# Kernel tuning notes

Measured on AMD Instinct MI355X. Metric: run time of the kernel, lower is better.

The kernel has to match this reference:

```python
import jax, jax.numpy as jnp
import numpy as np

B, S, LATENT = 256, 64, 20
U_DIM = LATENT // 5            # 4
T_HID, T_DEPTH = 20, 4         # treatment MLP
D_HID, D_DEPTH = 4 * LATENT, 4 # drift MLP (80 hidden)
T_LEN = 41
DT = 0.05
SIGMA, THETA, MU = 0.5, 1.0, 0.0
N = B * S
DIM_AUG = LATENT + 2           # latent + logqp + Tx


def _mlp(x, w_in, b_in, w_h, b_h, w_out, b_out, act):
    # input layer always ReLU (MLPSimple), hidden layers use `act`
    h = jax.nn.relu(x @ w_in.T + b_in)
    for i in range(w_h.shape[0]):
        h = act(h @ w_h[i].T + b_h[i])
    return h @ w_out.T + b_out


def setup_inputs() -> dict:
    key = jax.random.key(0)
    ks = jax.random.split(key, 20)

    def lin(k, out_d, in_d):
        bound = 1.0 / np.sqrt(in_d)
        return jax.random.uniform(k, (out_d, in_d), jnp.float32, -bound, bound)

    def bias(k, out_d, in_d):
        bound = 1.0 / np.sqrt(in_d)
        return jax.random.uniform(k, (out_d,), jnp.float32, -bound, bound)

    return {
        "z_SDE": jax.random.normal(ks[0], (B, S, LATENT), jnp.float32),
        "t": jnp.arange(T_LEN, dtype=jnp.float32) * DT,
        "Tx": jax.random.uniform(ks[1], (B,), jnp.float32),
        "noise": jax.random.normal(ks[2], (T_LEN - 1, N, DIM_AUG), jnp.float32),
        # treatment MLP: 1 -> 20 (ReLU) -> [20->20 ReLU]x4 -> 4
        "tw_in": lin(ks[3], T_HID, 1),
        "tb_in": bias(ks[4], T_HID, 1),
        "tw_h": jnp.stack([lin(jax.random.fold_in(ks[5], i), T_HID, T_HID) for i in range(T_DEPTH)]),
        "tb_h": jnp.stack([bias(jax.random.fold_in(ks[6], i), T_HID, T_HID) for i in range(T_DEPTH)]),
        "tw_out": lin(ks[7], U_DIM, T_HID),
        "tb_out": bias(ks[8], U_DIM, T_HID),
        # drift MLP: 24 -> 80 (ReLU) -> [80->80 Tanh]x4 -> 20
        "dw_in": lin(ks[9], D_HID, LATENT + U_DIM),
        "db_in": bias(ks[10], D_HID, LATENT + U_DIM),
        "dw_h": jnp.stack([lin(jax.random.fold_in(ks[11], i), D_HID, D_HID) for i in range(D_DEPTH)]),
        "db_h": jnp.stack([bias(jax.random.fold_in(ks[12], i), D_HID, D_HID) for i in range(D_DEPTH)]),
        "dw_out": lin(ks[13], LATENT, D_HID),
        "db_out": bias(ks[14], LATENT, D_HID),
    }


def reference(z_SDE, t, Tx, noise, tw_in, tb_in, tw_h, tb_h, tw_out, tb_out,
              dw_in, db_in, dw_h, db_h, dw_out, db_out):
    # build augmented initial state: [z, logqp0=0, Tx]  -> [N, DIM_AUG]
    Tx_rep = jnp.broadcast_to(Tx[:, None, None], (B, S, 1))
    aug_y0 = jnp.concatenate(
        [z_SDE, jnp.zeros((B, S, 1), z_SDE.dtype), Tx_rep.astype(z_SDE.dtype)], axis=-1
    ).reshape(N, DIM_AUG)

    dt = t[1] - t[0]           # 0.05, aligned with euler dt
    sqrt_dt = jnp.sqrt(dt)
    # diagonal diffusion: sigma on latent dims, 0 on (logqp, Tx) aug dims
    g_diag = jnp.concatenate([jnp.full((LATENT,), SIGMA, jnp.float32), jnp.zeros((2,), jnp.float32)])

    def f_aug(ti, y_aug):
        T_ = y_aug[:, -1]                     # treatment indicator
        y = y_aug[:, :LATENT]
        t_col = jnp.broadcast_to(ti, (N, 1)).astype(y.dtype)
        u = _mlp(t_col, tw_in, tb_in, tw_h, tb_h, tw_out, tb_out, jax.nn.relu)
        u_t = u * T_[:, None]
        h = THETA * (MU - y)                  # prior drift
        f = _mlp(jnp.concatenate([y, u_t], axis=-1), dw_in, db_in, dw_h, db_h, dw_out, db_out, jnp.tanh) - h
        # _stable_division(f - h, g); g = sigma = 0.5 > eps so plain division
        uu = (f - h) / SIGMA
        f_logqp = 0.5 * jnp.sum(uu * uu, axis=1, keepdims=True)
        return jnp.concatenate([f, f_logqp, jnp.zeros_like(f_logqp)], axis=1)

    def step(y, inp):
        ti, dW = inp
        y_new = y + f_aug(ti, y) * dt + g_diag[None, :] * (dW * sqrt_dt)
        return y_new, y_new

    _, ys_rest = jax.lax.scan(step, aug_y0, (t[:-1], noise))
    aug_ys = jnp.concatenate([aug_y0[None], ys_rest], axis=0)   # [T, N, DIM_AUG]
    # faithful to source: raw reshape of [T, N, dim] into [B, S, T, dim]
    aug_ys = aug_ys.reshape(-1, S, T_LEN, DIM_AUG)
    ys = aug_ys[:, :, :, :-2]
    logqp = aug_ys[:, :, -1, -2]
    return ys, logqp
```

## Files before the change

kernel.cpp:

```cpp
#include <hip/hip_runtime.h>
#include <math.h>
#include <stdint.h>

#define NPART 16384
#define NSTEP 40
#define DIMA  22
#define OUT0_ELEMS 13434880
#define TRAJ_OFF   160

typedef __attribute__((ext_vector_type(8))) short short8;
typedef __attribute__((ext_vector_type(4))) float floatx4;
typedef __attribute__((ext_vector_type(4))) int   intx4;
typedef __attribute__((ext_vector_type(2))) int   intx2;

union V4 { intx4 i; short8 s; floatx4 f; };

#define AIN_B   0
#define AH_B    5120
#define AOUT_B  56320
#define U_B     61440
#define LDS_BYTES 62080
#define STAGE_DW  15360

__device__ __forceinline__ uint32_t pk2(float a0, float a1) {
    uint32_t r;
    asm("v_cvt_pk_bf16_f32 %0, %1, %2" : "=v"(r) : "v"(a0), "v"(a1));
    return r;
}
__device__ __forceinline__ float fast_tanh(float x) {
    float e = __expf(2.0f * x);
    return 1.0f - 2.0f * __builtin_amdgcn_rcpf(e + 1.0f);
}

__global__ __launch_bounds__(256, 1) void sde_mfma(
    const float* __restrict__ z,      const float* __restrict__ t_arr,
    const float* __restrict__ Tx,     const float* __restrict__ noise,
    const float* __restrict__ dw_in,  const float* __restrict__ db_in,
    const float* __restrict__ dw_h,   const float* __restrict__ db_h,
    const float* __restrict__ dw_out, const float* __restrict__ db_out,
    const float* __restrict__ tw_in,  const float* __restrict__ tb_in,
    const float* __restrict__ tw_h,   const float* __restrict__ tb_h,
    const float* __restrict__ tw_out, const float* __restrict__ tb_out,
    float* __restrict__ out0,         float* __restrict__ traj)
{
    __shared__ __align__(16) uint8_t lds[LDS_BYTES];
    const int tid = threadIdx.x;

    for (int di = tid; di < STAGE_DW; di += 256) {
        uint32_t val = 0u;
        if (di < 1280) {
            int r = di & 255, lane = r >> 2, w = r & 3;
            int m = lane & 15, q = lane >> 4, mt = di >> 8;
            int f = -1;
            if (w < 2)            f = 4 * q + 2 * w;
            else if (q == 0)      f = 16 + 2 * (w - 2);
            else if (q == 1)      f = 20 + 2 * (w - 2);
            if (f >= 0)               val = pk2(dw_in[(mt * 16 + m) * 24 + f],
                                                dw_in[(mt * 16 + m) * 24 + f + 1]);
            else if (q == 2 && w == 2) val = pk2(db_in[mt * 16 + m], 0.f);
        } else if (di < 14080) {
            int q2 = di - 1280, g = q2 / 640, r = q2 % 640;
            int l = g / 5, mt = g % 5;
            int lane, f;
            if (r < 512) {
                int kt = r >> 8, rr = r & 255, w = rr & 3;
                lane = rr >> 2;
                f = 16 * (2 * kt + (w >> 1)) + 4 * (lane >> 4) + 2 * (w & 1);
            } else {
                int rr = r - 512, d = rr & 1;
                lane = rr >> 1;
                f = 64 + 4 * (lane >> 4) + 2 * d;
            }
            int m = lane & 15;
            val = pk2(dw_h[l * 6400 + (mt * 16 + m) * 80 + f],
                      dw_h[l * 6400 + (mt * 16 + m) * 80 + f + 1]);
        } else {
            int q2 = di - 14080, mt = q2 / 640, r = q2 % 640;
            int lane, f;
            if (r < 512) {
                int kt = r >> 8, rr = r & 255, w = rr & 3;
                lane = rr >> 2;
                f = 16 * (2 * kt + (w >> 1)) + 4 * (lane >> 4) + 2 * (w & 1);
            } else {
                int rr = r - 512, d = rr & 1;
                lane = rr >> 1;
                f = 64 + 4 * (lane >> 4) + 2 * d;
            }
            int m = mt * 16 + (lane & 15);
            if (m < 20) val = pk2(dw_out[m * 80 + f], dw_out[m * 80 + f + 1]);
        }
        ((uint32_t*)lds)[di] = val;
    }
    if (tid < NSTEP) {
        float ti = t_arr[tid];
        float hh[20], h2[20];
        #pragma unroll
        for (int j = 0; j < 20; j++) {
            float v = tw_in[j] * ti + tb_in[j];
            hh[j] = v > 0.f ? v : 0.f;
        }
        #pragma unroll
        for (int l = 0; l < 4; l++) {
            #pragma unroll
            for (int j = 0; j < 20; j++) {
                float a = tb_h[l * 20 + j];
                #pragma unroll
                for (int k = 0; k < 20; k++) a += tw_h[(l * 20 + j) * 20 + k] * hh[k];
                h2[j] = a > 0.f ? a : 0.f;
            }
            #pragma unroll
            for (int j = 0; j < 20; j++) hh[j] = h2[j];
        }
        #pragma unroll
        for (int c = 0; c < 4; c++) {
            float a = tb_out[c];
            #pragma unroll
            for (int k = 0; k < 20; k++) a += tw_out[c * 20 + k] * hh[k];
            ((float*)(lds + U_B))[tid * 4 + c] = a;
        }
    }

    const int lane = tid & 63;
    const int n15  = lane & 15;
    const int quad = lane >> 4;
    const int wv   = tid >> 6;
    const int n    = blockIdx.x * 64 + wv * 16 + n15;
    const float Txb = Tx[blockIdx.x];
    const float dtv = t_arr[1] - t_arr[0];
    const float sdt = sqrtf(dtv);
    const float hsdt = 0.5f * sdt;

    __syncthreads();

    V4 aIn[5];
    #pragma unroll
    for (int mt = 0; mt < 5; mt++)
        aIn[mt].i = *(const intx4*)(lds + AIN_B + mt * 1024 + lane * 16);

    V4 aH0[20], aH1[20], aH2[20];
    #pragma unroll
    for (int l = 0; l < 4; l++) {
        #pragma unroll
        for (int mt = 0; mt < 5; mt++) {
            const int g = l * 5 + mt;
            const uint8_t* grp = lds + AH_B + (size_t)g * 2560;
            aH0[g].i = *(const intx4*)(grp + lane * 16);
            aH1[g].i = *(const intx4*)(grp + 1024 + lane * 16);
            intx2 h2 = *(const intx2*)(grp + 2048 + lane * 8);
            uint32_t bd = (quad == 0) ? pk2(db_h[l * 80 + mt * 16 + n15], 0.f) : 0u;
            aH2[g].i = (intx4){h2[0], h2[1], (int)bd, 0};
        }
    }

    V4 aO0[2], aO1[2], aO2[2];
    #pragma unroll
    for (int mt = 0; mt < 2; mt++) {
        const uint8_t* grp = lds + AOUT_B + (size_t)mt * 2560;
        aO0[mt].i = *(const intx4*)(grp + lane * 16);
        aO1[mt].i = *(const intx4*)(grp + 1024 + lane * 16);
        intx2 h2 = *(const intx2*)(grp + 2048 + lane * 8);
        int m = mt * 16 + n15;
        uint32_t bd = (quad == 0 && m < 20) ? pk2(db_out[m], 0.f) : 0u;
        aO2[mt].i = (intx4){h2[0], h2[1], (int)bd, 0};
    }

    const floatx4 zf = {0.f, 0.f, 0.f, 0.f};

    float y0[4], y1[4] = {0.f, 0.f, 0.f, 0.f};
    {
        floatx4 zv = *(const floatx4*)(z + (size_t)n * 20 + quad * 4);
        #pragma unroll
        for (int r = 0; r < 4; r++) y0[r] = zv[r];
        *(floatx4*)(out0 + (size_t)n * 20 + quad * 4) = zv;
        if (quad == 0) {
            floatx4 z2 = *(const floatx4*)(z + (size_t)n * 20 + 16);
            #pragma unroll
            for (int r = 0; r < 4; r++) y1[r] = z2[r];
            *(floatx4*)(out0 + (size_t)n * 20 + 16) = z2;
            traj[n] = 0.f;
        }
    }

    floatx4 dW0n = *(const floatx4*)(noise + ((size_t)0 * NPART + n) * DIMA + quad * 4);
    floatx4 dW1n = *(const floatx4*)(noise + ((size_t)0 * NPART + n) * DIMA + 16);
    floatx4 uvn  = *(const floatx4*)((const float*)(lds + U_B));

    float lq = 0.f;
    for (int i = 0; i < NSTEP; i++) {
        floatx4 dW0 = dW0n, dW1 = dW1n, uv = uvn;
        if (i + 1 < NSTEP) {
            size_t nb2 = ((size_t)(i + 1) * NPART + n) * DIMA;
            dW0n = *(const floatx4*)(noise + nb2 + quad * 4);
            dW1n = *(const floatx4*)(noise + nb2 + 16);
            uvn  = *(const floatx4*)((const float*)(lds + U_B) + (i + 1) * 4);
        }

        float ut0 = uv[0] * Txb, ut1 = uv[1] * Txb;
        float ut2 = uv[2] * Txb, ut3 = uv[3] * Txb;

        V4 bin;
        bin.i[0] = pk2(y0[0], y0[1]);
        bin.i[1] = pk2(y0[2], y0[3]);
        if (quad == 0)      { bin.i[2] = pk2(y1[0], y1[1]); bin.i[3] = pk2(y1[2], y1[3]); }
        else if (quad == 1) { bin.i[2] = pk2(ut0, ut1);     bin.i[3] = pk2(ut2, ut3); }
        else if (quad == 2) { bin.i[2] = 0x00003F80;        bin.i[3] = 0; }
        else                { bin.i[2] = 0;                 bin.i[3] = 0; }

        floatx4 acc[5];
        #pragma unroll
        for (int mt = 0; mt < 5; mt++)
            acc[mt] = __builtin_amdgcn_mfma_f32_16x16x32_bf16(aIn[mt].s, bin.s, zf, 0, 0, 0);
        uint32_t pkA[5][2];
        #pragma unroll
        for (int mt = 0; mt < 5; mt++) {
            pkA[mt][0] = pk2(fmaxf(acc[mt][0], 0.f), fmaxf(acc[mt][1], 0.f));
            pkA[mt][1] = pk2(fmaxf(acc[mt][2], 0.f), fmaxf(acc[mt][3], 0.f));
        }

        #pragma unroll
        for (int l = 0; l < 4; l++) {
            V4 b0, b1, b2;
            b0.i = (intx4){(int)pkA[0][0], (int)pkA[0][1], (int)pkA[1][0], (int)pkA[1][1]};
            b1.i = (intx4){(int)pkA[2][0], (int)pkA[2][1], (int)pkA[3][0], (int)pkA[3][1]};
            b2.i = (intx4){(int)pkA[4][0], (int)pkA[4][1], 0x00003F80, 0};
            #pragma unroll
            for (int mt = 0; mt < 5; mt++) {
                const int g = l * 5 + mt;
                floatx4 c0 = __builtin_amdgcn_mfma_f32_16x16x32_bf16(aH0[g].s, b0.s, zf, 0, 0, 0);
                floatx4 c1 = __builtin_amdgcn_mfma_f32_16x16x32_bf16(aH1[g].s, b1.s, zf, 0, 0, 0);
                floatx4 c2 = __builtin_amdgcn_mfma_f32_16x16x32_bf16(aH2[g].s, b2.s, zf, 0, 0, 0);
                acc[mt] = (c0 + c1) + c2;
            }
            #pragma unroll
            for (int mt = 0; mt < 5; mt++) {
                pkA[mt][0] = pk2(fast_tanh(acc[mt][0]), fast_tanh(acc[mt][1]));
                pkA[mt][1] = pk2(fast_tanh(acc[mt][2]), fast_tanh(acc[mt][3]));
            }
        }

        V4 b0, b1, b2;
        b0.i = (intx4){(int)pkA[0][0], (int)pkA[0][1], (int)pkA[1][0], (int)pkA[1][1]};
        b1.i = (intx4){(int)pkA[2][0], (int)pkA[2][1], (int)pkA[3][0], (int)pkA[3][1]};
        b2.i = (intx4){(int)pkA[4][0], (int)pkA[4][1], 0x00003F80, 0};
        floatx4 oacc[2];
        #pragma unroll
        for (int mt = 0; mt < 2; mt++) {
            floatx4 c0 = __builtin_amdgcn_mfma_f32_16x16x32_bf16(aO0[mt].s, b0.s, zf, 0, 0, 0);
            floatx4 c1 = __builtin_amdgcn_mfma_f32_16x16x32_bf16(aO1[mt].s, b1.s, zf, 0, 0, 0);
            floatx4 c2 = __builtin_amdgcn_mfma_f32_16x16x32_bf16(aO2[mt].s, b2.s, zf, 0, 0, 0);
            oacc[mt] = (c0 + c1) + c2;
        }

        float part = 0.f;
        size_t obase = ((size_t)(i + 1) * NPART + n) * 20;
        floatx4 st;
        #pragma unroll
        for (int r = 0; r < 4; r++) {
            float o = oacc[0][r];
            float y = y0[r];
            float f = o + y;
            float uu = 2.f * o + 4.f * y;
            part += uu * uu;
            y0[r] = y + f * dtv + hsdt * dW0[r];
            st[r] = y0[r];
        }
        *(floatx4*)(out0 + obase + quad * 4) = st;
        if (quad == 0) {
            floatx4 st2;
            #pragma unroll
            for (int r = 0; r < 4; r++) {
                float o = oacc[1][r];
                float y = y1[r];
                float f = o + y;
                float uu = 2.f * o + 4.f * y;
                part += uu * uu;
                y1[r] = y + f * dtv + hsdt * dW1[r];
                st2[r] = y1[r];
            }
            *(floatx4*)(out0 + obase + 16) = st2;
        }
        part += __shfl_xor(part, 16);
        part += __shfl_xor(part, 32);
        lq += 0.5f * part * dtv;
        if (quad == 0) traj[(size_t)(i + 1) * NPART + n] = lq;
    }
}

__global__ void gather_logqp(const float* __restrict__ traj, float* __restrict__ out1) {
    int i = blockIdx.x * 256 + threadIdx.x;
    if (i < NPART) out1[i] = traj[(size_t)41 * i + 40];
}

extern "C" void kernel_launch(void* const* d_in, const int* in_sizes, int n_in,
                              void* d_out, int out_size, void* d_ws, size_t ws_size,
                              hipStream_t stream) {
    const float* z      = (const float*)d_in[0];
    const float* t_arr  = (const float*)d_in[1];
    const float* Tx     = (const float*)d_in[2];
    const float* noise  = (const float*)d_in[3];
    const float* tw_in  = (const float*)d_in[4];
    const float* tb_in  = (const float*)d_in[5];
    const float* tw_h   = (const float*)d_in[6];
    const float* tb_h   = (const float*)d_in[7];
    const float* tw_out = (const float*)d_in[8];
    const float* tb_out = (const float*)d_in[9];
    const float* dw_in  = (const float*)d_in[10];
    const float* db_in  = (const float*)d_in[11];
    const float* dw_h   = (const float*)d_in[12];
    const float* db_h   = (const float*)d_in[13];
    const float* dw_out = (const float*)d_in[14];
    const float* db_out = (const float*)d_in[15];

    float* wsf  = (float*)d_ws;
    float* traj = wsf + TRAJ_OFF;
    float* out0 = (float*)d_out;
    float* out1 = out0 + OUT0_ELEMS;

    hipLaunchKernelGGL(sde_mfma, dim3(256), dim3(256), 0, stream,
                       z, t_arr, Tx, noise, dw_in, db_in, dw_h, db_h,
                       dw_out, db_out, tw_in, tb_in, tw_h, tb_h, tw_out, tb_out,
                       out0, traj);
    hipLaunchKernelGGL(gather_logqp, dim3(64), dim3(256), 0, stream, traj, out1);
}
```

Before: 278.9 us.

## Split each particle group's drift MLP across two cooperating waves via LDS

The block grows from 256 to 512 threads. Each 16-particle group is now served by two waves: one computes 3 of the 5 hidden-output tiles, the other computes 2 tiles plus the output layer and the SDE update. The waves swap packed bf16 activations through double-buffered LDS with a barrier after each layer. The goal is to shorten each wave's serial MFMA and tanh chain and put two waves on each SIMD to hide latency. The cost is extra LDS traffic and six block-wide barriers per time step. MFMA partial sums are also chained through the accumulator instead of being added afterwards.

Result: faster. 254.1 us (-8.9%).

```diff
diff --git a/kernel.cpp b/kernel.cpp
--- a/kernel.cpp
+++ b/kernel.cpp
@@ -22,6 +22,10 @@
 #define LDS_BYTES 62080
 #define STAGE_DW  15360
 
+#define PAIR_STRIDE 6144
+#define ACT1_OFF    2560
+#define BIN_OFF     5120
+
 __device__ __forceinline__ uint32_t pk2(float a0, float a1) {
     uint32_t r;
     asm("v_cvt_pk_bf16_f32 %0, %1, %2" : "=v"(r) : "v"(a0), "v"(a1));
@@ -31,8 +35,21 @@
     float e = __expf(2.0f * x);
     return 1.0f - 2.0f * __builtin_amdgcn_rcpf(e + 1.0f);
 }
-
-__global__ __launch_bounds__(256, 1) void sde_mfma(
+__device__ __forceinline__ void relupk(floatx4 a, uint32_t& d0, uint32_t& d1) {
+    d0 = pk2(fmaxf(a[0], 0.f), fmaxf(a[1], 0.f));
+    d1 = pk2(fmaxf(a[2], 0.f), fmaxf(a[3], 0.f));
+}
+__device__ __forceinline__ void tanhpk(floatx4 a, uint32_t& d0, uint32_t& d1) {
+    d0 = pk2(fast_tanh(a[0]), fast_tanh(a[1]));
+    d1 = pk2(fast_tanh(a[2]), fast_tanh(a[3]));
+}
+__device__ __forceinline__ void pbar() {
+    asm volatile("s_waitcnt lgkmcnt(0)" ::: "memory");
+    __builtin_amdgcn_s_barrier();
+    asm volatile("" ::: "memory");
+}
+
+__global__ __launch_bounds__(512, 2) void sde_mfma(
     const float* __restrict__ z,      const float* __restrict__ t_arr,
     const float* __restrict__ Tx,     const float* __restrict__ noise,
     const float* __restrict__ dw_in,  const float* __restrict__ db_in,
@@ -46,7 +63,7 @@
     __shared__ __align__(16) uint8_t lds[LDS_BYTES];
     const int tid = threadIdx.x;
 
-    for (int di = tid; di < STAGE_DW; di += 256) {
+    for (int di = tid; di < STAGE_DW; di += 512) {
         uint32_t val = 0u;
         if (di < 1280) {
             int r = di & 255, lane = r >> 2, w = r & 3;
@@ -124,50 +141,73 @@
     const int n15  = lane & 15;
     const int quad = lane >> 4;
     const int wv   = tid >> 6;
-    const int n    = blockIdx.x * 64 + wv * 16 + n15;
+    const int pairid = wv & 3;
+    const bool roleB = (wv >= 4);
+    const int n    = blockIdx.x * 64 + pairid * 16 + n15;
     const float Txb = Tx[blockIdx.x];
     const float dtv = t_arr[1] - t_arr[0];
     const float sdt = sqrtf(dtv);
     const float hsdt = 0.5f * sdt;
 
+    uint8_t* const pb   = lds + pairid * PAIR_STRIDE;
+    uint32_t* const act0 = (uint32_t*)pb + lane;
+    uint32_t* const act1 = (uint32_t*)(pb + ACT1_OFF) + lane;
+    uint32_t* const binp = (uint32_t*)(pb + BIN_OFF) + lane;
+
     __syncthreads();
 
-    V4 aIn[5];
-    #pragma unroll
-    for (int mt = 0; mt < 5; mt++)
-        aIn[mt].i = *(const intx4*)(lds + AIN_B + mt * 1024 + lane * 16);
-
-    V4 aH0[20], aH1[20], aH2[20];
-    #pragma unroll
-    for (int l = 0; l < 4; l++) {
-        #pragma unroll
-        for (int mt = 0; mt < 5; mt++) {
-            const int g = l * 5 + mt;
-            const uint8_t* grp = lds + AH_B + (size_t)g * 2560;
+    V4 aIn[3], aH0[12], aH1[12], aH2[12];
+    if (!roleB) {
+        #pragma unroll
+        for (int mt = 0; mt < 3; mt++)
+            aIn[mt].i = *(const intx4*)(lds + AIN_B + mt * 1024 + lane * 16);
+        #pragma unroll
+        for (int l = 0; l < 4; l++) {
+            #pragma unroll
+            for (int mt = 0; mt < 3; mt++) {
+                const uint8_t* grp = lds + AH_B + (size_t)(l * 5 + mt) * 2560;
+                const int g = l * 3 + mt;
+                aH0[g].i = *(const intx4*)(grp + lane * 16);
+                aH1[g].i = *(const intx4*)(grp + 1024 + lane * 16);
+                intx2 h2 = *(const intx2*)(grp + 2048 + lane * 8);
+                uint32_t bd = (quad == 0) ? pk2(db_h[l * 80 + mt * 16 + n15], 0.f) : 0u;
+                aH2[g].i = (intx4){h2[0], h2[1], (int)bd, 0};
+            }
+        }
+    } else {
+        #pragma unroll
+        for (int mt = 0; mt < 2; mt++)
+            aIn[mt].i = *(const intx4*)(lds + AIN_B + (3 + mt) * 1024 + lane * 16);
+        #pragma unroll
+        for (int l = 0; l < 4; l++) {
+            #pragma unroll
+            for (int mt = 0; mt < 2; mt++) {
+                const uint8_t* grp = lds + AH_B + (size_t)(l * 5 + 3 + mt) * 2560;
+                const int g = l * 2 + mt;
+                aH0[g].i = *(const intx4*)(grp + lane * 16);
+                aH1[g].i = *(const intx4*)(grp + 1024 + lane * 16);
+                intx2 h2 = *(const intx2*)(grp + 2048 + lane * 8);
+                uint32_t bd = (quad == 0) ? pk2(db_h[l * 80 + (3 + mt) * 16 + n15], 0.f) : 0u;
+                aH2[g].i = (intx4){h2[0], h2[1], (int)bd, 0};
+            }
+        }
+        #pragma unroll
+        for (int mt = 0; mt < 2; mt++) {
+            const uint8_t* grp = lds + AOUT_B + (size_t)mt * 2560;
+            const int g = 8 + mt;
             aH0[g].i = *(const intx4*)(grp + lane * 16);
             aH1[g].i = *(const intx4*)(grp + 1024 + lane * 16);
             intx2 h2 = *(const intx2*)(grp + 2048 + lane * 8);
-            uint32_t bd = (quad == 0) ? pk2(db_h[l * 80 + mt * 16 + n15], 0.f) : 0u;
+            int m = mt * 16 + n15;
+            uint32_t bd = (quad == 0 && m < 20) ? pk2(db_out[m], 0.f) : 0u;
             aH2[g].i = (intx4){h2[0], h2[1], (int)bd, 0};
         }
     }
 
-    V4 aO0[2], aO1[2], aO2[2];
-    #pragma unroll
-    for (int mt = 0; mt < 2; mt++) {
-        const uint8_t* grp = lds + AOUT_B + (size_t)mt * 2560;
-        aO0[mt].i = *(const intx4*)(grp + lane * 16);
-        aO1[mt].i = *(const intx4*)(grp + 1024 + lane * 16);
-        intx2 h2 = *(const intx2*)(grp + 2048 + lane * 8);
-        int m = mt * 16 + n15;
-        uint32_t bd = (quad == 0 && m < 20) ? pk2(db_out[m], 0.f) : 0u;
-        aO2[mt].i = (intx4){h2[0], h2[1], (int)bd, 0};
-    }
-
-    const floatx4 zf = {0.f, 0.f, 0.f, 0.f};
-
-    float y0[4], y1[4] = {0.f, 0.f, 0.f, 0.f};
-    {
+    float y0[4] = {0.f, 0.f, 0.f, 0.f}, y1[4] = {0.f, 0.f, 0.f, 0.f};
+    V4 binB; binB.i = (intx4){0, 0, 0, 0};
+    float lq = 0.f;
+    if (roleB) {
         floatx4 zv = *(const floatx4*)(z + (size_t)n * 20 + quad * 4);
         #pragma unroll
         for (int r = 0; r < 4; r++) y0[r] = zv[r];
@@ -180,109 +220,164 @@
             traj[n] = 0.f;
         }
     }
-
-    floatx4 dW0n = *(const floatx4*)(noise + ((size_t)0 * NPART + n) * DIMA + quad * 4);
-    floatx4 dW1n = *(const floatx4*)(noise + ((size_t)0 * NPART + n) * DIMA + 16);
-    floatx4 uvn  = *(const floatx4*)((const float*)(lds + U_B));
-
-    float lq = 0.f;
+    __syncthreads();
+
+    if (roleB) {
+        const floatx4 uv0 = *(const floatx4*)((const float*)(lds + U_B));
+        float ut0 = uv0[0] * Txb, ut1 = uv0[1] * Txb;
+        float ut2 = uv0[2] * Txb, ut3 = uv0[3] * Txb;
+        binB.i[0] = pk2(y0[0], y0[1]);
+        binB.i[1] = pk2(y0[2], y0[3]);
+        if (quad == 0)      { binB.i[2] = pk2(y1[0], y1[1]); binB.i[3] = pk2(y1[2], y1[3]); }
+        else if (quad == 1) { binB.i[2] = pk2(ut0, ut1);     binB.i[3] = pk2(ut2, ut3); }
+        else if (quad == 2) { binB.i[2] = 0x00003F80;        binB.i[3] = 0; }
+        else                { binB.i[2] = 0;                 binB.i[3] = 0; }
+        binp[0] = binB.i[0]; binp[64] = binB.i[1];
+        binp[128] = binB.i[2]; binp[192] = binB.i[3];
+    }
+    __syncthreads();
+
+    const floatx4 zf = {0.f, 0.f, 0.f, 0.f};
+    floatx4 dW0 = zf, dW1 = zf, uvn = zf;
+    uint32_t pka[2], pkb[2], pkc[2];
+
     for (int i = 0; i < NSTEP; i++) {
-        floatx4 dW0 = dW0n, dW1 = dW1n, uv = uvn;
-        if (i + 1 < NSTEP) {
-            size_t nb2 = ((size_t)(i + 1) * NPART + n) * DIMA;
-            dW0n = *(const floatx4*)(noise + nb2 + quad * 4);
-            dW1n = *(const floatx4*)(noise + nb2 + 16);
-            uvn  = *(const floatx4*)((const float*)(lds + U_B) + (i + 1) * 4);
-        }
-
-        float ut0 = uv[0] * Txb, ut1 = uv[1] * Txb;
-        float ut2 = uv[2] * Txb, ut3 = uv[3] * Txb;
-
-        V4 bin;
-        bin.i[0] = pk2(y0[0], y0[1]);
-        bin.i[1] = pk2(y0[2], y0[3]);
-        if (quad == 0)      { bin.i[2] = pk2(y1[0], y1[1]); bin.i[3] = pk2(y1[2], y1[3]); }
-        else if (quad == 1) { bin.i[2] = pk2(ut0, ut1);     bin.i[3] = pk2(ut2, ut3); }
-        else if (quad == 2) { bin.i[2] = 0x00003F80;        bin.i[3] = 0; }
-        else                { bin.i[2] = 0;                 bin.i[3] = 0; }
-
-        floatx4 acc[5];
-        #pragma unroll
-        for (int mt = 0; mt < 5; mt++)
-            acc[mt] = __builtin_amdgcn_mfma_f32_16x16x32_bf16(aIn[mt].s, bin.s, zf, 0, 0, 0);
-        uint32_t pkA[5][2];
-        #pragma unroll
-        for (int mt = 0; mt < 5; mt++) {
-            pkA[mt][0] = pk2(fmaxf(acc[mt][0], 0.f), fmaxf(acc[mt][1], 0.f));
-            pkA[mt][1] = pk2(fmaxf(acc[mt][2], 0.f), fmaxf(acc[mt][3], 0.f));
-        }
+        if (roleB) {
+            size_t nb = ((size_t)i * NPART + n) * DIMA;
+            dW0 = *(const floatx4*)(noise + nb + quad * 4);
+            if (quad == 0) dW1 = *(const floatx4*)(noise + nb + 16);
+            int inx = (i + 1 < NSTEP) ? i + 1 : i;
+            uvn = *(const floatx4*)((const float*)(lds + U_B) + inx * 4);
+        }
+
+        if (!roleB) {
+            V4 binA;
+            binA.i = (intx4){(int)binp[0], (int)binp[64], (int)binp[128], (int)binp[192]};
+            floatx4 a0 = __builtin_amdgcn_mfma_f32_16x16x32_bf16(aIn[0].s, binA.s, zf, 0, 0, 0);
+            floatx4 a1 = __builtin_amdgcn_mfma_f32_16x16x32_bf16(aIn[1].s, binA.s, zf, 0, 0, 0);
+            floatx4 a2 = __builtin_amdgcn_mfma_f32_16x16x32_bf16(aIn[2].s, binA.s, zf, 0, 0, 0);
+            relupk(a0, pka[0], pka[1]);
+            relupk(a1, pkb[0], pkb[1]);
+            relupk(a2, pkc[0], pkc[1]);
+            act0[0]   = pka[0]; act0[64]  = pka[1];
+            act0[128] = pkb[0]; act0[192] = pkb[1];
+            act0[256] = pkc[0]; act0[320] = pkc[1];
+        } else {
+            floatx4 a0 = __builtin_amdgcn_mfma_f32_16x16x32_bf16(aIn[0].s, binB.s, zf, 0, 0, 0);
+            floatx4 a1 = __builtin_amdgcn_mfma_f32_16x16x32_bf16(aIn[1].s, binB.s, zf, 0, 0, 0);
+            relupk(a0, pka[0], pka[1]);
+            relupk(a1, pkb[0], pkb[1]);
+            act0[384] = pka[0]; act0[448] = pka[1];
+            act0[512] = pkb[0]; act0[576] = pkb[1];
+        }
+        pbar();
 
         #pragma unroll
         for (int l = 0; l < 4; l++) {
+            uint32_t* rb = (l & 1) ? act1 : act0;
+            uint32_t* wb = (l & 1) ? act0 : act1;
+            if (!roleB) {
+                uint32_t r6 = rb[384], r7 = rb[448], r8 = rb[512], r9 = rb[576];
+                V4 b0, b1, b2;
+                b0.i = (intx4){(int)pka[0], (int)pka[1], (int)pkb[0], (int)pkb[1]};
+                b1.i = (intx4){(int)pkc[0], (int)pkc[1], (int)r6, (int)r7};
+                b2.i = (intx4){(int)r8, (int)r9, 0x00003F80, 0};
+                floatx4 acc[3];
+                #pragma unroll
+                for (int mt = 0; mt < 3; mt++) {
+                    const int g = l * 3 + mt;
+                    floatx4 c = __builtin_amdgcn_mfma_f32_16x16x32_bf16(aH0[g].s, b0.s, zf, 0, 0, 0);
+                    c = __builtin_amdgcn_mfma_f32_16x16x32_bf16(aH1[g].s, b1.s, c, 0, 0, 0);
+                    acc[mt] = __builtin_amdgcn_mfma_f32_16x16x32_bf16(aH2[g].s, b2.s, c, 0, 0, 0);
+                }
+                tanhpk(acc[0], pka[0], pka[1]);
+                tanhpk(acc[1], pkb[0], pkb[1]);
+                tanhpk(acc[2], pkc[0], pkc[1]);
+                wb[0]   = pka[0]; wb[64]  = pka[1];
+                wb[128] = pkb[0]; wb[192] = pkb[1];
+                wb[256] = pkc[0]; wb[320] = pkc[1];
+            } else {
+                uint32_t r0 = rb[0], r1 = rb[64], r2 = rb[128], r3 = rb[192], r4 = rb[256], r5 = rb[320];
+                V4 b0, b1, b2;
+                b0.i = (intx4){(int)r0, (int)r1, (int)r2, (int)r3};
+                b1.i = (intx4){(int)r4, (int)r5, (int)pka[0], (int)pka[1]};
+                b2.i = (intx4){(int)pkb[0], (int)pkb[1], 0x00003F80, 0};
+                floatx4 acc[2];
+                #pragma unroll
+                for (int mt = 0; mt < 2; mt++) {
+                    const int g = l * 2 + mt;
+                    floatx4 c = __builtin_amdgcn_mfma_f32_16x16x32_bf16(aH0[g].s, b0.s, zf, 0, 0, 0);
+                    c = __builtin_amdgcn_mfma_f32_16x16x32_bf16(aH1[g].s, b1.s, c, 0, 0, 0);
+                    acc[mt] = __builtin_amdgcn_mfma_f32_16x16x32_bf16(aH2[g].s, b2.s, c, 0, 0, 0);
+                }
+                tanhpk(acc[0], pka[0], pka[1]);
+                tanhpk(acc[1], pkb[0], pkb[1]);
+                wb[384] = pka[0]; wb[448] = pka[1];
+                wb[512] = pkb[0]; wb[576] = pkb[1];
+            }
+            pbar();
+        }
+
+        if (roleB) {
+            uint32_t r0 = act0[0], r1 = act0[64], r2 = act0[128], r3 = act0[192], r4 = act0[256], r5 = act0[320];
             V4 b0, b1, b2;
-            b0.i = (intx4){(int)pkA[0][0], (int)pkA[0][1], (int)pkA[1][0], (int)pkA[1][1]};
-            b1.i = (intx4){(int)pkA[2][0], (int)pkA[2][1], (int)pkA[3][0], (int)pkA[3][1]};
-            b2.i = (intx4){(int)pkA[4][0], (int)pkA[4][1], 0x00003F80, 0};
-            #pragma unroll
-            for (int mt = 0; mt < 5; mt++) {
-                const int g = l * 5 + mt;
-                floatx4 c0 = __builtin_amdgcn_mfma_f32_16x16x32_bf16(aH0[g].s, b0.s, zf, 0, 0, 0);
-                floatx4 c1 = __builtin_amdgcn_mfma_f32_16x16x32_bf16(aH1[g].s, b1.s, zf, 0, 0, 0);
-                floatx4 c2 = __builtin_amdgcn_mfma_f32_16x16x32_bf16(aH2[g].s, b2.s, zf, 0, 0, 0);
-                acc[mt] = (c0 + c1) + c2;
-            }
-            #pragma unroll
-            for (int mt = 0; mt < 5; mt++) {
-                pkA[mt][0] = pk2(fast_tanh(acc[mt][0]), fast_tanh(acc[mt][1]));
-                pkA[mt][1] = pk2(fast_tanh(acc[mt][2]), fast_tanh(acc[mt][3]));
-            }
-        }
-
-        V4 b0, b1, b2;
-        b0.i = (intx4){(int)pkA[0][0], (int)pkA[0][1], (int)pkA[1][0], (int)pkA[1][1]};
-        b1.i = (intx4){(int)pkA[2][0], (int)pkA[2][1], (int)pkA[3][0], (int)pkA[3][1]};
-        b2.i = (intx4){(int)pkA[4][0], (int)pkA[4][1], 0x00003F80, 0};
-        floatx4 oacc[2];
-        #pragma unroll
-        for (int mt = 0; mt < 2; mt++) {
-            floatx4 c0 = __builtin_amdgcn_mfma_f32_16x16x32_bf16(aO0[mt].s, b0.s, zf, 0, 0, 0);
-            floatx4 c1 = __builtin_amdgcn_mfma_f32_16x16x32_bf16(aO1[mt].s, b1.s, zf, 0, 0, 0);
-            floatx4 c2 = __builtin_amdgcn_mfma_f32_16x16x32_bf16(aO2[mt].s, b2.s, zf, 0, 0, 0);
-            oacc[mt] = (c0 + c1) + c2;
-        }
-
-        float part = 0.f;
-        size_t obase = ((size_t)(i + 1) * NPART + n) * 20;
-        floatx4 st;
-        #pragma unroll
-        for (int r = 0; r < 4; r++) {
-            float o = oacc[0][r];
-            float y = y0[r];
-            float f = o + y;
-            float uu = 2.f * o + 4.f * y;
-            part += uu * uu;
-            y0[r] = y + f * dtv + hsdt * dW0[r];
-            st[r] = y0[r];
-        }
-        *(floatx4*)(out0 + obase + quad * 4) = st;
-        if (quad == 0) {
-            floatx4 st2;
+            b0.i = (intx4){(int)r0, (int)r1, (int)r2, (int)r3};
+            b1.i = (intx4){(int)r4, (int)r5, (int)pka[0], (int)pka[1]};
+            b2.i = (intx4){(int)pkb[0], (int)pkb[1], 0x00003F80, 0};
+            floatx4 oacc[2];
+            #pragma unroll
+            for (int mt = 0; mt < 2; mt++) {
+                const int g = 8 + mt;
+                floatx4 c = __builtin_amdgcn_mfma_f32_16x16x32_bf16(aH0[g].s, b0.s, zf, 0, 0, 0);
+                c = __builtin_amdgcn_mfma_f32_16x16x32_bf16(aH1[g].s, b1.s, c, 0, 0, 0);
+                oacc[mt] = __builtin_amdgcn_mfma_f32_16x16x32_bf16(aH2[g].s, b2.s, c, 0, 0, 0);
+            }
+
+            float part = 0.f;
+            size_t obase = ((size_t)(i + 1) * NPART + n) * 20;
+            floatx4 st;
             #pragma unroll
             for (int r = 0; r < 4; r++) {
-                float o = oacc[1][r];
-                float y = y1[r];
+                float o = oacc[0][r];
+                float y = y0[r];
                 float f = o + y;
                 float uu = 2.f * o + 4.f * y;
                 part += uu * uu;
-                y1[r] = y + f * dtv + hsdt * dW1[r];
-                st2[r] = y1[r];
-            }
-            *(floatx4*)(out0 + obase + 16) = st2;
-        }
-        part += __shfl_xor(part, 16);
-        part += __shfl_xor(part, 32);
-        lq += 0.5f * part * dtv;
-        if (quad == 0) traj[(size_t)(i + 1) * NPART + n] = lq;
+                y0[r] = y + f * dtv + hsdt * dW0[r];
+                st[r] = y0[r];
+            }
+            *(floatx4*)(out0 + obase + quad * 4) = st;
+            if (quad == 0) {
+                floatx4 st2;
+                #pragma unroll
+                for (int r = 0; r < 4; r++) {
+                    float o = oacc[1][r];
+                    float y = y1[r];
+                    float f = o + y;
+                    float uu = 2.f * o + 4.f * y;
+                    part += uu * uu;
+                    y1[r] = y + f * dtv + hsdt * dW1[r];
+                    st2[r] = y1[r];
+                }
+                *(floatx4*)(out0 + obase + 16) = st2;
+            }
+            part += __shfl_xor(part, 16);
+            part += __shfl_xor(part, 32);
+            lq += 0.5f * part * dtv;
+            if (quad == 0) traj[(size_t)(i + 1) * NPART + n] = lq;
+
+            float ut0 = uvn[0] * Txb, ut1 = uvn[1] * Txb;
+            float ut2 = uvn[2] * Txb, ut3 = uvn[3] * Txb;
+            binB.i[0] = pk2(y0[0], y0[1]);
+            binB.i[1] = pk2(y0[2], y0[3]);
+            if (quad == 0)      { binB.i[2] = pk2(y1[0], y1[1]); binB.i[3] = pk2(y1[2], y1[3]); }
+            else if (quad == 1) { binB.i[2] = pk2(ut0, ut1);     binB.i[3] = pk2(ut2, ut3); }
+            else if (quad == 2) { binB.i[2] = 0x00003F80;        binB.i[3] = 0; }
+            else                { binB.i[2] = 0;                 binB.i[3] = 0; }
+            binp[0] = binB.i[0]; binp[64] = binB.i[1];
+            binp[128] = binB.i[2]; binp[192] = binB.i[3];
+        }
+        pbar();
     }
 }
 
@@ -316,7 +411,7 @@
     float* out0 = (float*)d_out;
     float* out1 = out0 + OUT0_ELEMS;
 
-    hipLaunchKernelGGL(sde_mfma, dim3(256), dim3(256), 0, stream,
+    hipLaunchKernelGGL(sde_mfma, dim3(256), dim3(512), 0, stream,
                        z, t_arr, Tx, noise, dw_in, db_in, dw_h, db_h,
                        dw_out, db_out, tw_in, tb_in, tw_h, tb_h, tw_out, tb_out,
                        out0, traj);
```

## Interleave activation packing with chained MFMA accumulation across K-chunks

Applied to the files above, without the earlier changes.

Restructures each MLP layer so the three K-chunk MFMAs accumulate through the C operand instead of being summed with vector adds. Activation and packing of later K-chunks now run while earlier-chunk MFMAs are in flight, so VALU work overlaps the matrix pipeline. Also uses raw v_exp_f32 with a pre-scaled constant for tanh and moves noise prefetch and next-step input packing around. The deeper dependency chain per output tile may limit overlap, and the noise load is no longer prefetched a full step ahead.

New measurement: 274.4 us. About the same (-1.6%).

```diff
diff --git a/kernel.cpp b/kernel.cpp
--- a/kernel.cpp
+++ b/kernel.cpp
@@ -28,8 +28,18 @@
     return r;
 }
 __device__ __forceinline__ float fast_tanh(float x) {
-    float e = __expf(2.0f * x);
+    const float C = 2.0f * 1.44269504088896340736f;
+    float t = x * C, e;
+    asm("v_exp_f32 %0, %1" : "=v"(e) : "v"(t));
     return 1.0f - 2.0f * __builtin_amdgcn_rcpf(e + 1.0f);
+}
+__device__ __forceinline__ void relupk(floatx4 a, uint32_t& d0, uint32_t& d1) {
+    d0 = pk2(fmaxf(a[0], 0.f), fmaxf(a[1], 0.f));
+    d1 = pk2(fmaxf(a[2], 0.f), fmaxf(a[3], 0.f));
+}
+__device__ __forceinline__ void tanhpk(floatx4 a, uint32_t& d0, uint32_t& d1) {
+    d0 = pk2(fast_tanh(a[0]), fast_tanh(a[1]));
+    d1 = pk2(fast_tanh(a[2]), fast_tanh(a[3]));
 }
 
 __global__ __launch_bounds__(256, 1) void sde_mfma(
@@ -181,82 +191,77 @@
         }
     }
 
-    floatx4 dW0n = *(const floatx4*)(noise + ((size_t)0 * NPART + n) * DIMA + quad * 4);
-    floatx4 dW1n = *(const floatx4*)(noise + ((size_t)0 * NPART + n) * DIMA + 16);
-    floatx4 uvn  = *(const floatx4*)((const float*)(lds + U_B));
-
-    float lq = 0.f;
-    for (int i = 0; i < NSTEP; i++) {
-        floatx4 dW0 = dW0n, dW1 = dW1n, uv = uvn;
-        if (i + 1 < NSTEP) {
-            size_t nb2 = ((size_t)(i + 1) * NPART + n) * DIMA;
-            dW0n = *(const floatx4*)(noise + nb2 + quad * 4);
-            dW1n = *(const floatx4*)(noise + nb2 + 16);
-            uvn  = *(const floatx4*)((const float*)(lds + U_B) + (i + 1) * 4);
-        }
-
-        float ut0 = uv[0] * Txb, ut1 = uv[1] * Txb;
-        float ut2 = uv[2] * Txb, ut3 = uv[3] * Txb;
-
-        V4 bin;
+    V4 bin;
+    {
+        const floatx4 uv0 = *(const floatx4*)((const float*)(lds + U_B));
+        float ut0 = uv0[0] * Txb, ut1 = uv0[1] * Txb;
+        float ut2 = uv0[2] * Txb, ut3 = uv0[3] * Txb;
         bin.i[0] = pk2(y0[0], y0[1]);
         bin.i[1] = pk2(y0[2], y0[3]);
         if (quad == 0)      { bin.i[2] = pk2(y1[0], y1[1]); bin.i[3] = pk2(y1[2], y1[3]); }
         else if (quad == 1) { bin.i[2] = pk2(ut0, ut1);     bin.i[3] = pk2(ut2, ut3); }
         else if (quad == 2) { bin.i[2] = 0x00003F80;        bin.i[3] = 0; }
         else                { bin.i[2] = 0;                 bin.i[3] = 0; }
+    }
+
+    float lq = 0.f;
+    for (int i = 0; i < NSTEP; i++) {
+        size_t nbase = ((size_t)i * NPART + n) * DIMA;
+        floatx4 dW0 = *(const floatx4*)(noise + nbase + quad * 4);
+        floatx4 dW1 = *(const floatx4*)(noise + nbase + 16);
+        int inx = (i + 1 < NSTEP) ? i + 1 : i;
+        floatx4 uvn = *(const floatx4*)((const float*)(lds + U_B) + inx * 4);
 
         floatx4 acc[5];
         #pragma unroll
         for (int mt = 0; mt < 5; mt++)
             acc[mt] = __builtin_amdgcn_mfma_f32_16x16x32_bf16(aIn[mt].s, bin.s, zf, 0, 0, 0);
-        uint32_t pkA[5][2];
-        #pragma unroll
-        for (int mt = 0; mt < 5; mt++) {
-            pkA[mt][0] = pk2(fmaxf(acc[mt][0], 0.f), fmaxf(acc[mt][1], 0.f));
-            pkA[mt][1] = pk2(fmaxf(acc[mt][2], 0.f), fmaxf(acc[mt][3], 0.f));
-        }
-
+
+        uint32_t p0, p1, p2, p3, p4, p5, p6, p7, p8, p9;
+        V4 b0, b1, b2;
+        relupk(acc[0], p0, p1); relupk(acc[1], p2, p3);
+        b0.i = (intx4){(int)p0, (int)p1, (int)p2, (int)p3};
+
+        floatx4 nxt[5];
         #pragma unroll
         for (int l = 0; l < 4; l++) {
-            V4 b0, b1, b2;
-            b0.i = (intx4){(int)pkA[0][0], (int)pkA[0][1], (int)pkA[1][0], (int)pkA[1][1]};
-            b1.i = (intx4){(int)pkA[2][0], (int)pkA[2][1], (int)pkA[3][0], (int)pkA[3][1]};
-            b2.i = (intx4){(int)pkA[4][0], (int)pkA[4][1], 0x00003F80, 0};
-            #pragma unroll
-            for (int mt = 0; mt < 5; mt++) {
-                const int g = l * 5 + mt;
-                floatx4 c0 = __builtin_amdgcn_mfma_f32_16x16x32_bf16(aH0[g].s, b0.s, zf, 0, 0, 0);
-                floatx4 c1 = __builtin_amdgcn_mfma_f32_16x16x32_bf16(aH1[g].s, b1.s, zf, 0, 0, 0);
-                floatx4 c2 = __builtin_amdgcn_mfma_f32_16x16x32_bf16(aH2[g].s, b2.s, zf, 0, 0, 0);
-                acc[mt] = (c0 + c1) + c2;
-            }
-            #pragma unroll
-            for (int mt = 0; mt < 5; mt++) {
-                pkA[mt][0] = pk2(fast_tanh(acc[mt][0]), fast_tanh(acc[mt][1]));
-                pkA[mt][1] = pk2(fast_tanh(acc[mt][2]), fast_tanh(acc[mt][3]));
-            }
-        }
-
-        V4 b0, b1, b2;
-        b0.i = (intx4){(int)pkA[0][0], (int)pkA[0][1], (int)pkA[1][0], (int)pkA[1][1]};
-        b1.i = (intx4){(int)pkA[2][0], (int)pkA[2][1], (int)pkA[3][0], (int)pkA[3][1]};
-        b2.i = (intx4){(int)pkA[4][0], (int)pkA[4][1], 0x00003F80, 0};
-        floatx4 oacc[2];
-        #pragma unroll
-        for (int mt = 0; mt < 2; mt++) {
-            floatx4 c0 = __builtin_amdgcn_mfma_f32_16x16x32_bf16(aO0[mt].s, b0.s, zf, 0, 0, 0);
-            floatx4 c1 = __builtin_amdgcn_mfma_f32_16x16x32_bf16(aO1[mt].s, b1.s, zf, 0, 0, 0);
-            floatx4 c2 = __builtin_amdgcn_mfma_f32_16x16x32_bf16(aO2[mt].s, b2.s, zf, 0, 0, 0);
-            oacc[mt] = (c0 + c1) + c2;
-        }
+            #pragma unroll
+            for (int mt = 0; mt < 5; mt++)
+                nxt[mt] = __builtin_amdgcn_mfma_f32_16x16x32_bf16(aH0[l * 5 + mt].s, b0.s, zf, 0, 0, 0);
+            if (l == 0) { relupk(acc[2], p4, p5); relupk(acc[3], p6, p7); }
+            else        { tanhpk(acc[2], p4, p5); tanhpk(acc[3], p6, p7); }
+            b1.i = (intx4){(int)p4, (int)p5, (int)p6, (int)p7};
+            #pragma unroll
+            for (int mt = 0; mt < 5; mt++)
+                nxt[mt] = __builtin_amdgcn_mfma_f32_16x16x32_bf16(aH1[l * 5 + mt].s, b1.s, nxt[mt], 0, 0, 0);
+            if (l == 0) relupk(acc[4], p8, p9); else tanhpk(acc[4], p8, p9);
+            b2.i = (intx4){(int)p8, (int)p9, 0x00003F80, 0};
+            #pragma unroll
+            for (int mt = 0; mt < 5; mt++)
+                nxt[mt] = __builtin_amdgcn_mfma_f32_16x16x32_bf16(aH2[l * 5 + mt].s, b2.s, nxt[mt], 0, 0, 0);
+            #pragma unroll
+            for (int mt = 0; mt < 5; mt++) acc[mt] = nxt[mt];
+            tanhpk(acc[0], p0, p1); tanhpk(acc[1], p2, p3);
+            b0.i = (intx4){(int)p0, (int)p1, (int)p2, (int)p3};
+        }
+
+        floatx4 o0 = __builtin_amdgcn_mfma_f32_16x16x32_bf16(aO0[0].s, b0.s, zf, 0, 0, 0);
+        floatx4 o1 = __builtin_amdgcn_mfma_f32_16x16x32_bf16(aO0[1].s, b0.s, zf, 0, 0, 0);
+        tanhpk(acc[2], p4, p5); tanhpk(acc[3], p6, p7);
+        b1.i = (intx4){(int)p4, (int)p5, (int)p6, (int)p7};
+        o0 = __builtin_amdgcn_mfma_f32_16x16x32_bf16(aO1[0].s, b1.s, o0, 0, 0, 0);
+        o1 = __builtin_amdgcn_mfma_f32_16x16x32_bf16(aO1[1].s, b1.s, o1, 0, 0, 0);
+        tanhpk(acc[4], p8, p9);
+        b2.i = (intx4){(int)p8, (int)p9, 0x00003F80, 0};
+        o0 = __builtin_amdgcn_mfma_f32_16x16x32_bf16(aO2[0].s, b2.s, o0, 0, 0, 0);
+        o1 = __builtin_amdgcn_mfma_f32_16x16x32_bf16(aO2[1].s, b2.s, o1, 0, 0, 0);
 
         float part = 0.f;
         size_t obase = ((size_t)(i + 1) * NPART + n) * 20;
         floatx4 st;
         #pragma unroll
         for (int r = 0; r < 4; r++) {
-            float o = oacc[0][r];
+            float o = o0[r];
             float y = y0[r];
             float f = o + y;
             float uu = 2.f * o + 4.f * y;
@@ -269,7 +274,7 @@
             floatx4 st2;
             #pragma unroll
             for (int r = 0; r < 4; r++) {
-                float o = oacc[1][r];
+                float o = o1[r];
                 float y = y1[r];
                 float f = o + y;
                 float uu = 2.f * o + 4.f * y;
@@ -279,6 +284,18 @@
             }
             *(floatx4*)(out0 + obase + 16) = st2;
         }
+
+        {
+            float ut0 = uvn[0] * Txb, ut1 = uvn[1] * Txb;
+            float ut2 = uvn[2] * Txb, ut3 = uvn[3] * Txb;
+            bin.i[0] = pk2(y0[0], y0[1]);
+            bin.i[1] = pk2(y0[2], y0[3]);
+            if (quad == 0)      { bin.i[2] = pk2(y1[0], y1[1]); bin.i[3] = pk2(y1[2], y1[3]); }
+            else if (quad == 1) { bin.i[2] = pk2(ut0, ut1);     bin.i[3] = pk2(ut2, ut3); }
+            else if (quad == 2) { bin.i[2] = 0x00003F80;        bin.i[3] = 0; }
+            else                { bin.i[2] = 0;                 bin.i[3] = 0; }
+        }
+
         part += __shfl_xor(part, 16);
         part += __shfl_xor(part, 32);
         lq += 0.5f * part * dtv;
```
